# Kernel tuning notes

Hardware: AMD Instinct MI355X
Metric: run time of the kernel (lower is better)

The kernel has to match this reference:

```python
import jax, jax.numpy as jnp
import numpy as np

B, S, V, E = 64, 32, 50000, 300
H, D = 16, 16            # head_num, head_dim; model dim M = H*D = 256
M = H * D
AH = 200                 # attn_hidden_dim


def setup_inputs() -> dict:
    key = jax.random.key(0)
    ks = jax.random.split(key, 16)
    f = jnp.float32
    inp = {
        "x": jax.random.randint(ks[0], (B, S), 0, V),
        "emb": jax.random.normal(ks[1], (V, E), f) * 0.05,
        "W_proj": jax.random.normal(ks[2], (E, M), f) * 0.05,
        "b_proj": jnp.zeros((M,), f),
        "Wq": jax.random.normal(ks[3], (M, M), f) * 0.05,
        "bq": jnp.zeros((M,), f),
        "Wk": jax.random.normal(ks[4], (M, M), f) * 0.05,
        "bk": jnp.zeros((M,), f),
        "Wv": jax.random.normal(ks[5], (M, M), f) * 0.05,
        "bv": jnp.zeros((M,), f),
        "W_attn": jax.random.normal(ks[6], (2 * D, AH), f) * 0.05,  # attn_fc: 2*head_dim -> AH
        "b_attn": jnp.zeros((AH,), f),
        "attn_v": jax.random.normal(ks[7], (AH,), f),
        "W_fc": jax.random.normal(ks[8], (S * D, M), f) * 0.05,     # lazy fc: context.size(-1)=S*D -> M
        "b_fc": jnp.zeros((M,), f),
    }
    return inp


def reference(x, emb, W_proj, b_proj, Wq, bq, Wk, bk, Wv, bv,
              W_attn, b_attn, attn_v, W_fc, b_fc):
    # embedding + projection (300 -> 256); dropout = identity (eval)
    h = emb[x]                                   # [B,S,E]
    h = h @ W_proj + b_proj                      # [B,S,M]

    q = (h @ Wq + bq).reshape(B, S, H, D)        # [B,S,H,D]
    k = (h @ Wk + bk).reshape(B, S, H, D)
    v = (h @ Wv + bv).reshape(B, S, H, D)

    # attn_fc(concat(q_i, k_j)) = q_i @ W1 + k_j @ W2 + b  (exact same math, no concat)
    W1, W2 = W_attn[:D], W_attn[D:]              # each [D,AH]
    aq = jnp.einsum('bihd,de->bihe', q, W1)      # [B,S,H,AH]
    ak = jnp.einsum('bjhd,de->bjhe', k, W2)      # [B,S,H,AH]
    hid = jnp.tanh(aq[:, :, None] + ak[:, None, :] + b_attn)   # [B,S,S,H,AH]
    scores = jnp.einsum('bijhe,e->bijh', hid, attn_v)          # [B,S,S,H]

    w = jax.nn.softmax(scores, axis=2)           # softmax over key dim (dim=2)

    # torch.matmul([B,S,S,H], [B,S,H,D]) -> [B,S,S,D]: heads contracted, v at QUERY pos
    ctx = jnp.einsum('bijh,bihd->bijd', w, v)    # [B,S,S,D]
    ctx = ctx.reshape(B, S, S * D)               # [B,S,S*D]

    out = ctx @ W_fc + b_fc                      # [B,S,M]
    return out.max(axis=1)                       # AdaptiveMaxPool1d(1) over seq -> [B,M]
```

## Files before the change

kernel.cpp:

```cpp
#include <hip/hip_runtime.h>

#define B 64
#define S 32
#define V 50000
#define E 300
#define H 16
#define D 16
#define M 256
#define AH 200
#define AHH 100
#define BS 2048

#define C2 2.88539008177793f
#define LOG2E 1.44269504088896f

#if __has_builtin(__builtin_amdgcn_exp2f)
#define EXP2(x) __builtin_amdgcn_exp2f(x)
#else
#define EXP2(x) __builtin_exp2f(x)
#endif

__global__ __launch_bounds__(1024) void k1_embed_qkv(
    const int* __restrict__ x, const float* __restrict__ emb,
    const float* __restrict__ W_proj, const float* __restrict__ b_proj,
    const float* __restrict__ Wq, const float* __restrict__ bq,
    const float* __restrict__ Wk, const float* __restrict__ bk,
    const float* __restrict__ Wv, const float* __restrict__ bv,
    float* __restrict__ q, float* __restrict__ k, float* __restrict__ v)
{
    __shared__ float embl[8][E];
    __shared__ float hl[8][M];
    __shared__ float part[8][8][M];
    __shared__ int idxl[8];
    const int tid = threadIdx.x;
    const int col2 = (tid & 127) * 2;
    const int grp = tid >> 7;
    const int r0 = blockIdx.x * 8;
    const int rr = tid >> 7;
    const int rc2 = (tid & 127) * 2;

    if (tid < 8) idxl[tid] = x[r0 + tid];
    __syncthreads();
    for (int t = tid; t < 8 * E; t += 1024) {
        int r = t / E, e = t % E;
        embl[r][e] = emb[(long)idxl[r] * E + e];
    }
    __syncthreads();

    if (grp < 6) {
        float2 acc[8];
#pragma unroll
        for (int r = 0; r < 8; r++) acc[r] = make_float2(0.f, 0.f);
        const int e0 = 50 * grp;
#pragma unroll 4
        for (int e = e0; e < e0 + 50; e += 2) {
            float2 w0 = *reinterpret_cast<const float2*>(&W_proj[e * M + col2]);
            float2 w1 = *reinterpret_cast<const float2*>(&W_proj[(e + 1) * M + col2]);
#pragma unroll
            for (int r = 0; r < 8; r++) {
                float2 hm = *reinterpret_cast<const float2*>(&embl[r][e]);
                acc[r].x += hm.x * w0.x; acc[r].y += hm.x * w0.y;
                acc[r].x += hm.y * w1.x; acc[r].y += hm.y * w1.y;
            }
        }
#pragma unroll
        for (int r = 0; r < 8; r++)
            *reinterpret_cast<float2*>(&part[grp][r][col2]) = acc[r];
    }
    __syncthreads();
    {
        float2 s = *reinterpret_cast<const float2*>(&b_proj[rc2]);
#pragma unroll
        for (int g = 0; g < 6; g++) {
            float2 p = *reinterpret_cast<const float2*>(&part[g][rr][rc2]);
            s.x += p.x; s.y += p.y;
        }
        *reinterpret_cast<float2*>(&hl[rr][rc2]) = s;
    }
    __syncthreads();

    float2 aq[8], ak[8], av[8];
#pragma unroll
    for (int r = 0; r < 8; r++) {
        aq[r] = make_float2(0.f, 0.f);
        ak[r] = make_float2(0.f, 0.f);
        av[r] = make_float2(0.f, 0.f);
    }
    {
        const int cb = 32 * grp;
#pragma unroll 2
        for (int c = cb; c < cb + 32; c += 2) {
            float2 wq0 = *reinterpret_cast<const float2*>(&Wq[c * M + col2]);
            float2 wk0 = *reinterpret_cast<const float2*>(&Wk[c * M + col2]);
            float2 wv0 = *reinterpret_cast<const float2*>(&Wv[c * M + col2]);
            float2 wq1 = *reinterpret_cast<const float2*>(&Wq[(c + 1) * M + col2]);
            float2 wk1 = *reinterpret_cast<const float2*>(&Wk[(c + 1) * M + col2]);
            float2 wv1 = *reinterpret_cast<const float2*>(&Wv[(c + 1) * M + col2]);
#pragma unroll
            for (int r = 0; r < 8; r++) {
                float2 hm = *reinterpret_cast<const float2*>(&hl[r][c]);
                aq[r].x += hm.x * wq0.x; aq[r].y += hm.x * wq0.y;
                ak[r].x += hm.x * wk0.x; ak[r].y += hm.x * wk0.y;
                av[r].x += hm.x * wv0.x; av[r].y += hm.x * wv0.y;
                aq[r].x += hm.y * wq1.x; aq[r].y += hm.y * wq1.y;
                ak[r].x += hm.y * wk1.x; ak[r].y += hm.y * wk1.y;
                av[r].x += hm.y * wv1.x; av[r].y += hm.y * wv1.y;
            }
        }
    }
#pragma unroll
    for (int r = 0; r < 8; r++)
        *reinterpret_cast<float2*>(&part[grp][r][col2]) = aq[r];
    __syncthreads();
    {
        float2 s = *reinterpret_cast<const float2*>(&bq[rc2]);
#pragma unroll
        for (int g = 0; g < 8; g++) {
            float2 p = *reinterpret_cast<const float2*>(&part[g][rr][rc2]);
            s.x += p.x; s.y += p.y;
        }
        *reinterpret_cast<float2*>(&q[(r0 + rr) * M + rc2]) = s;
    }
    __syncthreads();
#pragma unroll
    for (int r = 0; r < 8; r++)
        *reinterpret_cast<float2*>(&part[grp][r][col2]) = ak[r];
    __syncthreads();
    {
        float2 s = *reinterpret_cast<const float2*>(&bk[rc2]);
#pragma unroll
        for (int g = 0; g < 8; g++) {
            float2 p = *reinterpret_cast<const float2*>(&part[g][rr][rc2]);
            s.x += p.x; s.y += p.y;
        }
        *reinterpret_cast<float2*>(&k[(r0 + rr) * M + rc2]) = s;
    }
    __syncthreads();
#pragma unroll
    for (int r = 0; r < 8; r++)
        *reinterpret_cast<float2*>(&part[grp][r][col2]) = av[r];
    __syncthreads();
    {
        float2 s = *reinterpret_cast<const float2*>(&bv[rc2]);
#pragma unroll
        for (int g = 0; g < 8; g++) {
            float2 p = *reinterpret_cast<const float2*>(&part[g][rr][rc2]);
            s.x += p.x; s.y += p.y;
        }
        *reinterpret_cast<float2*>(&v[(r0 + rr) * M + rc2]) = s;
    }
}

#define EQS 104
#define EKS 34
__global__ __launch_bounds__(512, 8) void k2_scores(
    const float* __restrict__ q, const float* __restrict__ k,
    const float* __restrict__ W_attn, const float* __restrict__ b_attn,
    const float* __restrict__ attn_v, float* __restrict__ psc)
{
    __shared__ __align__(16) float ql[S][D];
    __shared__ __align__(16) float kl[S][D];
    __shared__ __align__(16) float Eqs[S][EQS];
    __shared__ __align__(16) float Ekts[AHH][EKS];
    const int tid = threadIdx.x;
    const int eh = blockIdx.x & 1;
    const int h = (blockIdx.x >> 1) & 15;
    const int b = blockIdx.x >> 5;
    const int e0g = eh * AHH;

    ql[tid >> 4][tid & 15] = q[(b * S + (tid >> 4)) * M + h * D + (tid & 15)];
    kl[tid >> 4][tid & 15] = k[(b * S + (tid >> 4)) * M + h * D + (tid & 15)];
    __syncthreads();

    {
        const int e = tid & 127;
        const int pg = tid >> 7;
        if (e < AHH) {
            const int eg = e0g + e;
            if (pg < 2) {
                float w1c[D];
#pragma unroll
                for (int d = 0; d < D; d++) w1c[d] = W_attn[d * AH + eg];
                float be = b_attn[eg];
                const int i0 = pg * 16;
                for (int i = i0; i < i0 + 16; i++) {
                    float a1 = be;
                    const float4* qr = reinterpret_cast<const float4*>(&ql[i][0]);
#pragma unroll
                    for (int dq = 0; dq < 4; dq++) {
                        float4 qv = qr[dq];
                        a1 += qv.x * w1c[4 * dq] + qv.y * w1c[4 * dq + 1]
                            + qv.z * w1c[4 * dq + 2] + qv.w * w1c[4 * dq + 3];
                    }
                    Eqs[i][e] = EXP2(C2 * a1);
                }
            } else {
                float w2c[D];
#pragma unroll
                for (int d = 0; d < D; d++) w2c[d] = W_attn[(D + d) * AH + eg];
                const int j0i = (pg - 2) * 16;
                for (int j = j0i; j < j0i + 16; j++) {
                    float a2 = 0.f;
                    const float4* kr = reinterpret_cast<const float4*>(&kl[j][0]);
#pragma unroll
                    for (int dq = 0; dq < 4; dq++) {
                        float4 kv = kr[dq];
                        a2 += kv.x * w2c[4 * dq] + kv.y * w2c[4 * dq + 1]
                            + kv.z * w2c[4 * dq + 2] + kv.w * w2c[4 * dq + 3];
                    }
                    Ekts[e][j] = EXP2(C2 * a2);
                }
            }
        }
    }
    __syncthreads();

    const int i = tid >> 4;
    const int j0 = tid & 15;
    float acc0 = 0.f, acc1 = 0.f;
    const float4* avp = reinterpret_cast<const float4*>(attn_v + e0g);
#pragma unroll 1
    for (int ec = 0; ec < AHH / 4; ec++) {
        float4 eq = *reinterpret_cast<const float4*>(&Eqs[i][4 * ec]);
        float4 avv = avp[ec];
        float2 e0 = *reinterpret_cast<const float2*>(&Ekts[4 * ec + 0][2 * j0]);
        float2 e1 = *reinterpret_cast<const float2*>(&Ekts[4 * ec + 1][2 * j0]);
        float2 e2 = *reinterpret_cast<const float2*>(&Ekts[4 * ec + 2][2 * j0]);
        float2 e3 = *reinterpret_cast<const float2*>(&Ekts[4 * ec + 3][2 * j0]);
        {
            float a0 = 1.f + eq.x * e0.x, a1 = 1.f + eq.y * e1.x;
            float a2 = 1.f + eq.z * e2.x, a3 = 1.f + eq.w * e3.x;
            float p01 = a0 * a1, p23 = a2 * a3;
            float t01 = avv.x * a1 + avv.y * a0;
            float t23 = avv.z * a3 + avv.w * a2;
            float num = t01 * p23 + t23 * p01;
            acc0 += num * __builtin_amdgcn_rcpf(p01 * p23);
        }
        {
            float a0 = 1.f + eq.x * e0.y, a1 = 1.f + eq.y * e1.y;
            float a2 = 1.f + eq.z * e2.y, a3 = 1.f + eq.w * e3.y;
            float p01 = a0 * a1, p23 = a2 * a3;
            float t01 = avv.x * a1 + avv.y * a0;
            float t23 = avv.z * a3 + avv.w * a2;
            float num = t01 * p23 + t23 * p01;
            acc1 += num * __builtin_amdgcn_rcpf(p01 * p23);
        }
    }
    float2 out2 = make_float2(-2.f * acc0, -2.f * acc1);
    float* po = psc + (size_t)eh * (B * H * S * S);
    *reinterpret_cast<float2*>(&po[((b * H + h) * S + i) * S + 2 * j0]) = out2;
}

__global__ __launch_bounds__(1024) void k3_ctx_fc(
    const float* __restrict__ v, const float* __restrict__ psc,
    const float* __restrict__ W_fc, const float* __restrict__ b_fc,
    float* __restrict__ part_out)
{
    __shared__ float vl[8][H][D];
    __shared__ __align__(16) float wl[H][8][S];
    __shared__ float ctxl[8][S * D];
    __shared__ float pfc[4][8][M];
    const int tid = threadIdx.x;
    const int b = blockIdx.x >> 2, ig = blockIdx.x & 3;
    const float* psc0 = psc;
    const float* psc1 = psc + (size_t)(B * H * S * S);

    for (int t = tid; t < 8 * M; t += 1024) {
        int i = t >> 8, md = t & 255;
        vl[i][md >> 4][md & 15] = v[(b * S + ig * 8 + i) * M + md];
    }
    for (int t = tid; t < H * 8 * S; t += 1024) {
        int h = t >> 8, r = t & 255;
        int i = r >> 5, j = r & 31;
        int idx = ((b * H + h) * S + (ig * 8 + i)) * S + j;
        wl[h][i][j] = psc0[idx] + psc1[idx];
    }
    __syncthreads();

    {
        const int row = tid >> 3;
        const int h = row >> 3, il = row & 7;
        const int jq = (tid & 7) * 4;
        float4 sv = *reinterpret_cast<const float4*>(&wl[h][il][jq]);
        float mx = fmaxf(fmaxf(sv.x, sv.y), fmaxf(sv.z, sv.w));
#pragma unroll
        for (int msk = 1; msk < 8; msk <<= 1) mx = fmaxf(mx, __shfl_xor(mx, msk, 64));
        float p0 = EXP2(LOG2E * (sv.x - mx));
        float p1 = EXP2(LOG2E * (sv.y - mx));
        float p2 = EXP2(LOG2E * (sv.z - mx));
        float p3 = EXP2(LOG2E * (sv.w - mx));
        float ps = p0 + p1 + p2 + p3;
#pragma unroll
        for (int msk = 1; msk < 8; msk <<= 1) ps += __shfl_xor(ps, msk, 64);
        float rs = __builtin_amdgcn_rcpf(ps);
        float4 wv = make_float4(p0 * rs, p1 * rs, p2 * rs, p3 * rs);
        *reinterpret_cast<float4*>(&wl[h][il][jq]) = wv;
    }
    __syncthreads();

    for (int t = tid; t < 8 * S * D; t += 1024) {
        int i = t >> 9, jd = t & 511;
        int j = jd >> 4, d = jd & 15;
        float a = 0.f;
#pragma unroll
        for (int h = 0; h < H; h++) a += wl[h][i][j] * vl[i][h][d];
        ctxl[i][j * D + d] = a;
    }
    __syncthreads();

    const int col = tid & 255, grp = tid >> 8;
    {
        float acc[8];
#pragma unroll
        for (int ii = 0; ii < 8; ii++) acc[ii] = 0.f;
        const int e0 = 128 * grp;
#pragma unroll 4
        for (int e = e0; e < e0 + 128; e++) {
            float wf = W_fc[e * M + col];
#pragma unroll
            for (int ii = 0; ii < 8; ii++) acc[ii] += ctxl[ii][e] * wf;
        }
#pragma unroll
        for (int ii = 0; ii < 8; ii++) pfc[grp][ii][col] = acc[ii];
    }
    __syncthreads();
    if (tid < 256) {
        float bf = b_fc[tid];
        float mxv = -3.4e38f;
#pragma unroll
        for (int ii = 0; ii < 8; ii++) {
            float s = pfc[0][ii][tid] + pfc[1][ii][tid] + pfc[2][ii][tid]
                    + pfc[3][ii][tid] + bf;
            mxv = fmaxf(mxv, s);
        }
        part_out[(b * 4 + ig) * M + tid] = mxv;
    }
}

__global__ __launch_bounds__(256) void k4_max(
    const float* __restrict__ part, float* __restrict__ out)
{
    const int b = blockIdx.x, m = threadIdx.x;
    float v0 = part[(b * 4 + 0) * M + m];
    float v1 = part[(b * 4 + 1) * M + m];
    float v2 = part[(b * 4 + 2) * M + m];
    float v3 = part[(b * 4 + 3) * M + m];
    out[b * M + m] = fmaxf(fmaxf(v0, v1), fmaxf(v2, v3));
}

extern "C" void kernel_launch(void* const* d_in, const int* in_sizes, int n_in,
                              void* d_out, int out_size, void* d_ws, size_t ws_size,
                              hipStream_t stream) {
    const int*   x      = (const int*)  d_in[0];
    const float* emb    = (const float*)d_in[1];
    const float* W_proj = (const float*)d_in[2];
    const float* b_proj = (const float*)d_in[3];
    const float* Wq     = (const float*)d_in[4];
    const float* bq     = (const float*)d_in[5];
    const float* Wk     = (const float*)d_in[6];
    const float* bk     = (const float*)d_in[7];
    const float* Wv     = (const float*)d_in[8];
    const float* bv     = (const float*)d_in[9];
    const float* W_attn = (const float*)d_in[10];
    const float* b_attn = (const float*)d_in[11];
    const float* attn_v = (const float*)d_in[12];
    const float* W_fc   = (const float*)d_in[13];
    const float* b_fc   = (const float*)d_in[14];
    float* out = (float*)d_out;

    float* ws   = (float*)d_ws;
    float* q    = ws;
    float* k    = q + BS * M;
    float* v    = k + BS * M;
    float* psc  = v + BS * M;
    float* part = psc + 2 * B * H * S * S;

    k1_embed_qkv<<<BS / 8, 1024, 0, stream>>>(x, emb, W_proj, b_proj,
                                              Wq, bq, Wk, bk, Wv, bv, q, k, v);
    k2_scores<<<B * H * 2, 512, 0, stream>>>(q, k, W_attn, b_attn, attn_v, psc);
    k3_ctx_fc<<<B * 4, 1024, 0, stream>>>(v, psc, W_fc, b_fc, part);
    k4_max<<<B, 256, 0, stream>>>(part, out);
}
```

Measured before the change: 84.16 us.

## Transpose key-exp table and split AH loop across thread pairs in score kernel

The key-side exponential table is stored j-major instead of e-major, so each thread reads float4 vectors of four consecutive e values for four keys. Each thread now computes four key positions over half of the e-chunks, and pairs of threads combine partial sums with a cross-lane shuffle before each writes two outputs. This aims to cut LDS load instructions per FLOP and add instruction-level parallelism with four independent accumulators. In exchange it adds shuffle traffic and higher register use, and the new LDS access pattern may cause bank conflicts.

```diff
diff --git a/kernel.cpp b/kernel.cpp
--- a/kernel.cpp
+++ b/kernel.cpp
@@ -152,7 +152,7 @@
 }
 
 #define EQS 104
-#define EKS 34
+#define EKJS 100
 __global__ __launch_bounds__(512, 8) void k2_scores(
     const float* __restrict__ q, const float* __restrict__ k,
     const float* __restrict__ W_attn, const float* __restrict__ b_attn,
@@ -161,7 +161,7 @@
     __shared__ __align__(16) float ql[S][D];
     __shared__ __align__(16) float kl[S][D];
     __shared__ __align__(16) float Eqs[S][EQS];
-    __shared__ __align__(16) float Ekts[AHH][EKS];
+    __shared__ __align__(16) float Ektj[S][EKJS];
     const int tid = threadIdx.x;
     const int eh = blockIdx.x & 1;
     const int h = (blockIdx.x >> 1) & 15;
@@ -208,7 +208,7 @@
                         a2 += kv.x * w2c[4 * dq] + kv.y * w2c[4 * dq + 1]
                             + kv.z * w2c[4 * dq + 2] + kv.w * w2c[4 * dq + 3];
                     }
-                    Ekts[e][j] = EXP2(C2 * a2);
+                    Ektj[j][e] = EXP2(C2 * a2);
                 }
             }
         }
@@ -216,39 +216,45 @@
     __syncthreads();
 
     const int i = tid >> 4;
-    const int j0 = tid & 15;
-    float acc0 = 0.f, acc1 = 0.f;
+    const int jq = (tid >> 1) & 7;
+    const int es = tid & 1;
+    const int jb = 4 * jq;
+    float acc0 = 0.f, acc1 = 0.f, acc2 = 0.f, acc3 = 0.f;
     const float4* avp = reinterpret_cast<const float4*>(attn_v + e0g);
-#pragma unroll 1
-    for (int ec = 0; ec < AHH / 4; ec++) {
+#pragma unroll 2
+    for (int ec = es; ec < AHH / 4; ec += 2) {
         float4 eq = *reinterpret_cast<const float4*>(&Eqs[i][4 * ec]);
         float4 avv = avp[ec];
-        float2 e0 = *reinterpret_cast<const float2*>(&Ekts[4 * ec + 0][2 * j0]);
-        float2 e1 = *reinterpret_cast<const float2*>(&Ekts[4 * ec + 1][2 * j0]);
-        float2 e2 = *reinterpret_cast<const float2*>(&Ekts[4 * ec + 2][2 * j0]);
-        float2 e3 = *reinterpret_cast<const float2*>(&Ekts[4 * ec + 3][2 * j0]);
-        {
-            float a0 = 1.f + eq.x * e0.x, a1 = 1.f + eq.y * e1.x;
-            float a2 = 1.f + eq.z * e2.x, a3 = 1.f + eq.w * e3.x;
-            float p01 = a0 * a1, p23 = a2 * a3;
-            float t01 = avv.x * a1 + avv.y * a0;
-            float t23 = avv.z * a3 + avv.w * a2;
-            float num = t01 * p23 + t23 * p01;
-            acc0 += num * __builtin_amdgcn_rcpf(p01 * p23);
-        }
-        {
-            float a0 = 1.f + eq.x * e0.y, a1 = 1.f + eq.y * e1.y;
-            float a2 = 1.f + eq.z * e2.y, a3 = 1.f + eq.w * e3.y;
-            float p01 = a0 * a1, p23 = a2 * a3;
-            float t01 = avv.x * a1 + avv.y * a0;
-            float t23 = avv.z * a3 + avv.w * a2;
-            float num = t01 * p23 + t23 * p01;
-            acc1 += num * __builtin_amdgcn_rcpf(p01 * p23);
-        }
-    }
-    float2 out2 = make_float2(-2.f * acc0, -2.f * acc1);
+        float4 k0 = *reinterpret_cast<const float4*>(&Ektj[jb + 0][4 * ec]);
+        float4 k1 = *reinterpret_cast<const float4*>(&Ektj[jb + 1][4 * ec]);
+        float4 k2v = *reinterpret_cast<const float4*>(&Ektj[jb + 2][4 * ec]);
+        float4 k3v = *reinterpret_cast<const float4*>(&Ektj[jb + 3][4 * ec]);
+#define RAT4(kv, accv)                                                        \
+        {                                                                     \
+            float a0 = 1.f + eq.x * kv.x, a1 = 1.f + eq.y * kv.y;             \
+            float a2 = 1.f + eq.z * kv.z, a3 = 1.f + eq.w * kv.w;             \
+            float p01 = a0 * a1, p23 = a2 * a3;                               \
+            float t01 = avv.x * a1 + avv.y * a0;                              \
+            float t23 = avv.z * a3 + avv.w * a2;                              \
+            float num = t01 * p23 + t23 * p01;                                \
+            accv += num * __builtin_amdgcn_rcpf(p01 * p23);                   \
+        }
+        RAT4(k0, acc0)
+        RAT4(k1, acc1)
+        RAT4(k2v, acc2)
+        RAT4(k3v, acc3)
+#undef RAT4
+    }
+    acc0 += __shfl_xor(acc0, 1, 64);
+    acc1 += __shfl_xor(acc1, 1, 64);
+    acc2 += __shfl_xor(acc2, 1, 64);
+    acc3 += __shfl_xor(acc3, 1, 64);
+
     float* po = psc + (size_t)eh * (B * H * S * S);
-    *reinterpret_cast<float2*>(&po[((b * H + h) * S + i) * S + 2 * j0]) = out2;
+    float2 out2 = (es == 0) ? make_float2(-2.f * acc0, -2.f * acc1)
+                            : make_float2(-2.f * acc2, -2.f * acc3);
+    *reinterpret_cast<float2*>(
+        &po[((b * H + h) * S + i) * S + jb + 2 * es]) = out2;
 }
 
 __global__ __launch_bounds__(1024) void k3_ctx_fc(
```

Result: slower. 88.22 us (+4.8%).

## Register-tile k2 score loop 4x4 over (i,j) and split AH across lanes

Applied to the files above, without the earlier changes.

Rewrites the score accumulation in k2 so each thread computes a 4x4 tile of (query,key) pairs over a strided subset of the hidden dimension, then reduces across 8 lanes with xor shuffles. The key exponentials are stored row-major per key and attn_v is staged in shared memory, so each thread reuses its loaded Eq/Ek float4 values across 4 rows and 4 columns. The aim is fewer LDS loads per arithmetic operation. The cost is more registers (launch bounds lowered from 8 to 6 waves), extra shuffles, and only half the lanes doing the store.

```diff
diff --git a/kernel.cpp b/kernel.cpp
--- a/kernel.cpp
+++ b/kernel.cpp
@@ -152,8 +152,8 @@
 }
 
 #define EQS 104
-#define EKS 34
-__global__ __launch_bounds__(512, 8) void k2_scores(
+#define EKS 104
+__global__ __launch_bounds__(512, 6) void k2_scores(
     const float* __restrict__ q, const float* __restrict__ k,
     const float* __restrict__ W_attn, const float* __restrict__ b_attn,
     const float* __restrict__ attn_v, float* __restrict__ psc)
@@ -161,7 +161,8 @@
     __shared__ __align__(16) float ql[S][D];
     __shared__ __align__(16) float kl[S][D];
     __shared__ __align__(16) float Eqs[S][EQS];
-    __shared__ __align__(16) float Ekts[AHH][EKS];
+    __shared__ __align__(16) float Ekj[S][EKS];
+    __shared__ __align__(16) float avl[AHH];
     const int tid = threadIdx.x;
     const int eh = blockIdx.x & 1;
     const int h = (blockIdx.x >> 1) & 15;
@@ -170,6 +171,7 @@
 
     ql[tid >> 4][tid & 15] = q[(b * S + (tid >> 4)) * M + h * D + (tid & 15)];
     kl[tid >> 4][tid & 15] = k[(b * S + (tid >> 4)) * M + h * D + (tid & 15)];
+    if (tid < AHH) avl[tid] = attn_v[e0g + tid];
     __syncthreads();
 
     {
@@ -208,47 +210,70 @@
                         a2 += kv.x * w2c[4 * dq] + kv.y * w2c[4 * dq + 1]
                             + kv.z * w2c[4 * dq + 2] + kv.w * w2c[4 * dq + 3];
                     }
-                    Ekts[e][j] = EXP2(C2 * a2);
+                    Ekj[j][e] = EXP2(C2 * a2);
                 }
             }
         }
     }
     __syncthreads();
 
-    const int i = tid >> 4;
-    const int j0 = tid & 15;
-    float acc0 = 0.f, acc1 = 0.f;
-    const float4* avp = reinterpret_cast<const float4*>(attn_v + e0g);
-#pragma unroll 1
-    for (int ec = 0; ec < AHH / 4; ec++) {
-        float4 eq = *reinterpret_cast<const float4*>(&Eqs[i][4 * ec]);
-        float4 avv = avp[ec];
-        float2 e0 = *reinterpret_cast<const float2*>(&Ekts[4 * ec + 0][2 * j0]);
-        float2 e1 = *reinterpret_cast<const float2*>(&Ekts[4 * ec + 1][2 * j0]);
-        float2 e2 = *reinterpret_cast<const float2*>(&Ekts[4 * ec + 2][2 * j0]);
-        float2 e3 = *reinterpret_cast<const float2*>(&Ekts[4 * ec + 3][2 * j0]);
-        {
-            float a0 = 1.f + eq.x * e0.x, a1 = 1.f + eq.y * e1.x;
-            float a2 = 1.f + eq.z * e2.x, a3 = 1.f + eq.w * e3.x;
-            float p01 = a0 * a1, p23 = a2 * a3;
-            float t01 = avv.x * a1 + avv.y * a0;
-            float t23 = avv.z * a3 + avv.w * a2;
-            float num = t01 * p23 + t23 * p01;
-            acc0 += num * __builtin_amdgcn_rcpf(p01 * p23);
-        }
-        {
-            float a0 = 1.f + eq.x * e0.y, a1 = 1.f + eq.y * e1.y;
-            float a2 = 1.f + eq.z * e2.y, a3 = 1.f + eq.w * e3.y;
-            float p01 = a0 * a1, p23 = a2 * a3;
-            float t01 = avv.x * a1 + avv.y * a0;
-            float t23 = avv.z * a3 + avv.w * a2;
-            float num = t01 * p23 + t23 * p01;
-            acc1 += num * __builtin_amdgcn_rcpf(p01 * p23);
-        }
-    }
-    float2 out2 = make_float2(-2.f * acc0, -2.f * acc1);
-    float* po = psc + (size_t)eh * (B * H * S * S);
-    *reinterpret_cast<float2*>(&po[((b * H + h) * S + i) * S + 2 * j0]) = out2;
+    const int eg = tid & 7;
+    const int jb = (tid >> 3) & 7;
+    const int ib = tid >> 6;
+    const int rq = 4 * ib;
+    const int rk = 4 * jb;
+    float acc[4][4];
+#pragma unroll
+    for (int i = 0; i < 4; i++)
+#pragma unroll
+        for (int j = 0; j < 4; j++) acc[i][j] = 0.f;
+
+    for (int ec = eg; ec < AHH / 4; ec += 8) {
+        const int c = 4 * ec;
+        float4 avv = *reinterpret_cast<const float4*>(&avl[c]);
+        float4 eq0 = *reinterpret_cast<const float4*>(&Eqs[rq + 0][c]);
+        float4 eq1 = *reinterpret_cast<const float4*>(&Eqs[rq + 1][c]);
+        float4 eq2 = *reinterpret_cast<const float4*>(&Eqs[rq + 2][c]);
+        float4 eq3 = *reinterpret_cast<const float4*>(&Eqs[rq + 3][c]);
+#pragma unroll
+        for (int jr = 0; jr < 4; jr++) {
+            float4 ek = *reinterpret_cast<const float4*>(&Ekj[rk + jr][c]);
+#define RAT4(eqv, accv)                                                       \
+            {                                                                 \
+                float a0 = 1.f + eqv.x * ek.x, a1 = 1.f + eqv.y * ek.y;       \
+                float a2 = 1.f + eqv.z * ek.z, a3 = 1.f + eqv.w * ek.w;       \
+                float p01 = a0 * a1, p23 = a2 * a3;                           \
+                float t01 = avv.x * a1 + avv.y * a0;                          \
+                float t23 = avv.z * a3 + avv.w * a2;                          \
+                float num = t01 * p23 + t23 * p01;                            \
+                accv += num * __builtin_amdgcn_rcpf(p01 * p23);               \
+            }
+            RAT4(eq0, acc[0][jr])
+            RAT4(eq1, acc[1][jr])
+            RAT4(eq2, acc[2][jr])
+            RAT4(eq3, acc[3][jr])
+#undef RAT4
+        }
+    }
+
+#pragma unroll
+    for (int i = 0; i < 4; i++)
+#pragma unroll
+        for (int j = 0; j < 4; j++) {
+            float a = acc[i][j];
+            a += __shfl_xor(a, 1, 64);
+            a += __shfl_xor(a, 2, 64);
+            a += __shfl_xor(a, 4, 64);
+            acc[i][j] = a;
+        }
+
+    if (eg < 4) {
+        float* po = psc + (size_t)eh * (B * H * S * S);
+        float4 o = make_float4(-2.f * acc[eg][0], -2.f * acc[eg][1],
+                               -2.f * acc[eg][2], -2.f * acc[eg][3]);
+        *reinterpret_cast<float4*>(
+            &po[((b * H + h) * S + (rq + eg)) * S + rk]) = o;
+    }
 }
 
 __global__ __launch_bounds__(1024) void k3_ctx_fc(
```

Result: slower. 93.84 us (+11.5%).
